# Performance work log

Hardware: AMD Instinct MI355X
Metric: run time of the kernel (lower is better)

Reference implementation:

```python
import jax, jax.numpy as jnp
import numpy as np

HID = 256
NUM_ENT = 100000
NUM_REL = 50
E = 320000  # edges per direction; edge_index has 2*E columns
BN_EPS = 1e-5


def setup_inputs() -> dict:
    key = jax.random.key(0)
    ks = jax.random.split(key, 10)
    x = jax.random.normal(ks[0], (NUM_ENT, HID), dtype=jnp.float32)
    edge_index = jax.random.randint(ks[1], (2, 2 * E), 0, NUM_ENT)
    edge_type = jax.random.randint(ks[2], (2 * E,), 0, NUM_REL)
    rel_embed = jax.random.normal(ks[3], (NUM_REL, HID), dtype=jnp.float32)
    # xavier_normal init: std = sqrt(2 / (fan_in + fan_out))
    w_std = (2.0 / (HID + HID)) ** 0.5
    w_loop = jax.random.normal(ks[4], (HID, HID), dtype=jnp.float32) * w_std
    w_in = jax.random.normal(ks[5], (HID, HID), dtype=jnp.float32) * w_std
    w_out = jax.random.normal(ks[6], (HID, HID), dtype=jnp.float32) * w_std
    w_rel = jax.random.normal(ks[7], (HID, HID), dtype=jnp.float32) * w_std
    loop_rel = jax.random.normal(ks[8], (1, HID), dtype=jnp.float32) * ((2.0 / (1 + HID)) ** 0.5)
    bn_weight = jnp.ones((HID,), dtype=jnp.float32)
    bn_bias = jnp.zeros((HID,), dtype=jnp.float32)
    return {
        "x": x, "edge_index": edge_index, "edge_type": edge_type,
        "rel_embed": rel_embed, "w_loop": w_loop, "w_in": w_in,
        "w_out": w_out, "w_rel": w_rel, "loop_rel": loop_rel,
        "bn_weight": bn_weight, "bn_bias": bn_bias,
    }


def _compute_norm(edge_index, num_ent):
    # symmetric D^-1/2 * D^-1/2 norm; degree counted on row (target) index
    row, col = edge_index[0], edge_index[1]
    deg = jax.ops.segment_sum(jnp.ones_like(row, dtype=jnp.float32), row, num_segments=num_ent)
    deg_inv = jnp.where(deg > 0, deg ** -0.5, 0.0)
    return deg_inv[row] * deg_inv[col]


def _propagate(x, idx, etype, rel_all, W, norm, num_ent):
    # gather source nodes (idx[1]), compose with relation emb (mult), transform, scale, scatter-add to targets (idx[0])
    msg = (x[idx[1]] * rel_all[etype]) @ W  # [E, d]
    if norm is not None:
        msg = msg * norm[:, None]
    return jax.ops.segment_sum(msg, idx[0], num_segments=num_ent)


def reference(x, edge_index, edge_type, rel_embed, w_loop, w_in, w_out, w_rel,
              loop_rel, bn_weight, bn_bias):
    num_ent = x.shape[0]
    rel_all = jnp.concatenate([rel_embed, loop_rel], axis=0)  # [R+1, d]
    e = edge_index.shape[1] // 2
    in_index, out_index = edge_index[:, :e], edge_index[:, e:]
    in_type, out_type = edge_type[:e], edge_type[e:]

    in_norm = _compute_norm(in_index, num_ent)
    out_norm = _compute_norm(out_index, num_ent)

    in_res = _propagate(x, in_index, in_type, rel_all, w_in, in_norm, num_ent)
    out_res = _propagate(x, out_index, out_type, rel_all, w_out, out_norm, num_ent)
    # self-loop: identity scatter -> just per-node compose+transform
    loop_res = (x * loop_rel) @ w_loop

    out = (in_res + out_res + loop_res) * (1.0 / 3.0)

    # BatchNorm1d in training mode (batch stats, biased variance)
    mean = out.mean(axis=0)
    var = out.var(axis=0)
    out = (out - mean) * jax.lax.rsqrt(var + BN_EPS) * bn_weight + bn_bias

    rel_out = (rel_all @ w_rel)[:-1]  # drop loop relation
    return out, rel_out
```

## Files before the change

### kernel.cpp

```cpp
#include <hip/hip_runtime.h>

#define HID     256
#define N_ENT   100000
#define TOT_E   640000
#define HALF_E  320000
#define NSEG    (2 * N_ENT)
#define BN_EPSF 1e-5f
#define SCAN_ELEMS 1024
#define NBLK_SCAN  ((NSEG + SCAN_ELEMS - 1) / SCAN_ELEMS)

typedef short bf16x8 __attribute__((ext_vector_type(8)));
typedef short bf16x4 __attribute__((ext_vector_type(4)));
typedef float f32x4  __attribute__((ext_vector_type(4)));

__device__ __forceinline__ short f2b(float f) {
    union { float f; unsigned u; } c; c.f = f;
    unsigned u = c.u;
    u += 0x7FFF + ((u >> 16) & 1);
    return (short)(u >> 16);
}
__device__ __forceinline__ float b2f(short b) {
    union { unsigned u; float f; } c;
    c.u = ((unsigned)(unsigned short)b) << 16;
    return c.f;
}

#define NX8 (N_ENT * HID / 8)
#define NR8 (50 * HID / 8)
#define CONV_BLOCKS ((NX8 + NR8 + 255) / 256)
__global__ void prep_kernel(const float* __restrict__ x, short* __restrict__ xh,
                            const float* __restrict__ rel, short* __restrict__ relh,
                            const float* __restrict__ w_in, const float* __restrict__ w_out,
                            const float* __restrict__ w_loop, const float* __restrict__ loop_rel,
                            short* __restrict__ WT,
                            int* __restrict__ offs, float* __restrict__ stats) {
    int bid = blockIdx.x;
    int tid = threadIdx.x;
    if (bid < CONV_BLOCKS) {
        int i = bid * 256 + tid;
        if (i < NSEG) offs[i] = 0;
        if (i < 512) stats[i] = 0.f;
        const float* src; short* dst; int idx;
        if (i < NX8) { src = x; dst = xh; idx = i; }
        else if (i < NX8 + NR8) { src = rel; dst = relh; idx = i - NX8; }
        else return;
        const float4* p = (const float4*)(src + (size_t)idx * 8);
        float4 v0 = p[0], v1 = p[1];
        bf16x8 pk;
        pk[0]=f2b(v0.x); pk[1]=f2b(v0.y); pk[2]=f2b(v0.z); pk[3]=f2b(v0.w);
        pk[4]=f2b(v1.x); pk[5]=f2b(v1.y); pk[6]=f2b(v1.z); pk[7]=f2b(v1.w);
        *(bf16x8*)(dst + (size_t)idx * 8) = pk;
    } else {
        int n = bid - CONV_BLOCKS;
        int t = tid;
        float v0 = w_in  [(size_t)t * HID + n];
        float v1 = w_out [(size_t)t * HID + n];
        float v2 = w_loop[(size_t)t * HID + n] * loop_rel[t];
        short* row = WT + (size_t)n * 768;
        row[t]       = f2b(v0);
        row[256 + t] = f2b(v1);
        row[512 + t] = f2b(v2);
    }
}

__global__ void hist_kernel(const int* __restrict__ ei, int* __restrict__ offs) {
    int j = blockIdx.x * 256 + threadIdx.x;
    if (j >= TOT_E) return;
    int seg = ei[j] + ((j < HALF_E) ? 0 : N_ENT);
    atomicAdd(&offs[seg], 1);
}

__global__ __launch_bounds__(256) void scan1(int* __restrict__ offs, int* __restrict__ bsums,
                                             float* __restrict__ rnorm) {
    __shared__ int tsum[256];
    int b = blockIdx.x, t = threadIdx.x;
    int base = b * SCAN_ELEMS + t * 4;
    int v[4] = {0, 0, 0, 0};
    if (base + 3 < NSEG) {
        int4 lv = *(const int4*)(offs + base);
        v[0] = lv.x; v[1] = lv.y; v[2] = lv.z; v[3] = lv.w;
    } else {
        for (int i = 0; i < 4; ++i) if (base + i < NSEG) v[i] = offs[base + i];
    }
    #pragma unroll
    for (int i = 0; i < 4; ++i)
        if (base + i < NSEG)
            rnorm[base + i] = (v[i] > 0) ? rsqrtf((float)v[i]) : 0.f;
    tsum[t] = v[0] + v[1] + v[2] + v[3];
    __syncthreads();
    for (int d = 1; d < 256; d <<= 1) {
        int val = (t >= d) ? tsum[t - d] : 0;
        __syncthreads();
        tsum[t] += val;
        __syncthreads();
    }
    int run = (t == 0) ? 0 : tsum[t - 1];
    if (t == 255) bsums[b] = tsum[255];
    int w[4];
    for (int i = 0; i < 4; ++i) { w[i] = run; run += v[i]; }
    if (base + 3 < NSEG) *(int4*)(offs + base) = make_int4(w[0], w[1], w[2], w[3]);
    else for (int i = 0; i < 4; ++i) if (base + i < NSEG) offs[base + i] = w[i];
}

__global__ __launch_bounds__(256) void scan3f(int* __restrict__ offs, const int* __restrict__ bsums) {
    __shared__ int tmp[256];
    int b = blockIdx.x, t = threadIdx.x;
    tmp[t] = (t < NBLK_SCAN) ? bsums[t] : 0;
    __syncthreads();
    for (int d = 1; d < 256; d <<= 1) {
        int val = (t >= d) ? tmp[t - d] : 0;
        __syncthreads();
        tmp[t] += val;
        __syncthreads();
    }
    int add = (b == 0) ? 0 : tmp[b - 1];
    int base = b * SCAN_ELEMS + t * 4;
    if (base + 3 < NSEG) {
        int4 v = *(int4*)(offs + base);
        v.x += add; v.y += add; v.z += add; v.w += add;
        *(int4*)(offs + base) = v;
    } else {
        for (int i = 0; i < 4; ++i) if (base + i < NSEG) offs[base + i] += add;
    }
}

__global__ void fill8_kernel(const int* __restrict__ ei, const int* __restrict__ et,
                             int* __restrict__ offs, const float* __restrict__ rnorm,
                             int2* __restrict__ elist8) {
    int j = blockIdx.x * 256 + threadIdx.x;
    if (j >= TOT_E) return;
    int hb  = (j < HALF_E) ? 0 : N_ENT;
    int seg = ei[j] + hb;
    int col = ei[TOT_E + j];
    float norm = rnorm[seg] * rnorm[hb + col];
    int pos = atomicAdd(&offs[seg], 1);
    elist8[pos] = make_int2(col | (et[j] << 17), __float_as_int(norm));
}

__global__ __launch_bounds__(256) void gather_h(
        const short* __restrict__ xh, const short* __restrict__ relh,
        const int* __restrict__ offs, const int2* __restrict__ elist8,
        short* __restrict__ accA, short* __restrict__ accB) {
    int s = blockIdx.x * 4 + (threadIdx.x >> 6);
    int lane = threadIdx.x & 63;
    int start = (s == 0) ? 0 : offs[s - 1];
    int end   = offs[s];
    float ax0=0.f, ay0=0.f, az0=0.f, aw0=0.f;
    float ax1=0.f, ay1=0.f, az1=0.f, aw1=0.f;
    int e = start;
    for (; e + 2 <= end; e += 2) {
        int2 p0 = elist8[e];
        int2 p1 = elist8[e + 1];
        int   c0 = p0.x & 0x1FFFF, t0 = p0.x >> 17;
        float n0 = __int_as_float(p0.y);
        int   c1 = p1.x & 0x1FFFF, t1 = p1.x >> 17;
        float n1 = __int_as_float(p1.y);
        bf16x4 xv0 = *(const bf16x4*)(xh   + (size_t)c0 * HID + lane * 4);
        bf16x4 rv0 = *(const bf16x4*)(relh + (size_t)t0 * HID + lane * 4);
        bf16x4 xv1 = *(const bf16x4*)(xh   + (size_t)c1 * HID + lane * 4);
        bf16x4 rv1 = *(const bf16x4*)(relh + (size_t)t1 * HID + lane * 4);
        ax0 += b2f(xv0[0]) * b2f(rv0[0]) * n0;
        ay0 += b2f(xv0[1]) * b2f(rv0[1]) * n0;
        az0 += b2f(xv0[2]) * b2f(rv0[2]) * n0;
        aw0 += b2f(xv0[3]) * b2f(rv0[3]) * n0;
        ax1 += b2f(xv1[0]) * b2f(rv1[0]) * n1;
        ay1 += b2f(xv1[1]) * b2f(rv1[1]) * n1;
        az1 += b2f(xv1[2]) * b2f(rv1[2]) * n1;
        aw1 += b2f(xv1[3]) * b2f(rv1[3]) * n1;
    }
    if (e < end) {
        int2 p = elist8[e];
        int   c = p.x & 0x1FFFF, t = p.x >> 17;
        float n = __int_as_float(p.y);
        bf16x4 xv = *(const bf16x4*)(xh   + (size_t)c * HID + lane * 4);
        bf16x4 rv = *(const bf16x4*)(relh + (size_t)t * HID + lane * 4);
        ax0 += b2f(xv[0]) * b2f(rv[0]) * n;
        ay0 += b2f(xv[1]) * b2f(rv[1]) * n;
        az0 += b2f(xv[2]) * b2f(rv[2]) * n;
        aw0 += b2f(xv[3]) * b2f(rv[3]) * n;
    }
    int hb = (s >= N_ENT) ? N_ENT : 0;
    short* dst = ((s >= N_ENT) ? accB : accA) + (size_t)(s - hb) * HID + lane * 4;
    bf16x4 pk;
    pk[0] = f2b(ax0 + ax1); pk[1] = f2b(ay0 + ay1);
    pk[2] = f2b(az0 + az1); pk[3] = f2b(aw0 + aw1);
    *(bf16x4*)dst = pk;
}

template <bool BF16OUT>
__global__ __launch_bounds__(256, 4) void gemm_mfma_h(
        const short* __restrict__ accA, const short* __restrict__ accB,
        const short* __restrict__ xh, const short* __restrict__ WT,
        float* __restrict__ out, short* __restrict__ outh, float* __restrict__ stats)
{
    __shared__ __align__(16) short As[64 * 64];
    __shared__ __align__(16) short Bs[256 * 64];
    const int tid = threadIdx.x;
    const int l   = tid & 63;
    const int wid = tid >> 6;
    const int r0  = blockIdx.x * 64;
    const int lr  = l & 15;
    const int lg  = l >> 4;

    f32x4 acc[4][4];
    #pragma unroll
    for (int i = 0; i < 4; ++i)
        #pragma unroll
        for (int j = 0; j < 4; ++j)
            acc[i][j] = (f32x4){0.f, 0.f, 0.f, 0.f};

    const int sg = tid & 7;
    const int sr = tid >> 3;

    for (int kt = 0; kt < 12; ++kt) {
        const int src = kt >> 2;
        const short* Ap = (src == 0) ? accA : ((src == 1) ? accB : xh);
        const int ksg = kt * 64;
        const int ksl = (kt & 3) * 64;
        __syncthreads();
        #pragma unroll
        for (int h = 0; h < 2; ++h) {
            int r  = sr + 32 * h;
            int gr = r0 + r;
            bf16x8 v = {0,0,0,0,0,0,0,0};
            if (gr < N_ENT) v = *(const bf16x8*)(Ap + (size_t)gr * HID + ksl + sg * 8);
            *(bf16x8*)&As[r * 64 + ((sg ^ (r & 7)) << 3)] = v;
        }
        #pragma unroll
        for (int i = 0; i < 8; ++i) {
            int n = sr + 32 * i;
            bf16x8 w = *(const bf16x8*)(WT + (size_t)n * 768 + ksg + sg * 8);
            *(bf16x8*)&Bs[n * 64 + ((sg ^ (n & 7)) << 3)] = w;
        }
        __syncthreads();
        #pragma unroll
        for (int kc = 0; kc < 2; ++kc) {
            const int gsel = kc * 4 + lg;
            bf16x8 af[4];
            #pragma unroll
            for (int i = 0; i < 4; ++i) {
                int r = 16 * i + lr;
                af[i] = *(const bf16x8*)&As[r * 64 + ((gsel ^ (r & 7)) << 3)];
            }
            #pragma unroll
            for (int j = 0; j < 4; ++j) {
                int n = wid * 64 + 16 * j + lr;
                bf16x8 bfr = *(const bf16x8*)&Bs[n * 64 + ((gsel ^ (n & 7)) << 3)];
                #pragma unroll
                for (int i = 0; i < 4; ++i)
                    acc[i][j] = __builtin_amdgcn_mfma_f32_16x16x32_bf16(
                                    af[i], bfr, acc[i][j], 0, 0, 0);
            }
        }
    }

    const float third = 1.f / 3.f;
    float s[4]  = {0.f, 0.f, 0.f, 0.f};
    float sq[4] = {0.f, 0.f, 0.f, 0.f};
    #pragma unroll
    for (int i = 0; i < 4; ++i) {
        #pragma unroll
        for (int v = 0; v < 4; ++v) {
            int grow = r0 + 16 * i + lg * 4 + v;
            if (grow < N_ENT) {
                #pragma unroll
                for (int j = 0; j < 4; ++j) {
                    float val = acc[i][j][v] * third;
                    int col = wid * 64 + 16 * j + lr;
                    if (BF16OUT) outh[(size_t)grow * HID + col] = f2b(val);
                    else         out [(size_t)grow * HID + col] = val;
                    s[j] += val; sq[j] += val * val;
                }
            }
        }
    }
    #pragma unroll
    for (int j = 0; j < 4; ++j) {
        s[j]  += __shfl_xor(s[j], 16);  s[j]  += __shfl_xor(s[j], 32);
        sq[j] += __shfl_xor(sq[j], 16); sq[j] += __shfl_xor(sq[j], 32);
    }
    if (lg == 0) {
        #pragma unroll
        for (int j = 0; j < 4; ++j) {
            int c = wid * 64 + 16 * j + lr;
            atomicAdd(&stats[c], s[j]);
            atomicAdd(&stats[HID + c], sq[j]);
        }
    }
}

#define BN_BLOCKS 1024
__global__ void bn_relout_h(const short* __restrict__ outh, float* __restrict__ out,
                            const float* __restrict__ stats,
                            const float* __restrict__ bnw, const float* __restrict__ bnb,
                            const float* __restrict__ rel_embed, const float* __restrict__ w_rel,
                            float* __restrict__ rel_out) {
    if (blockIdx.x < BN_BLOCKS) {
        const float invN = 1.f / (float)N_ENT;
        const int total8 = N_ENT * (HID / 8);
        for (int i = blockIdx.x * 256 + threadIdx.x; i < total8; i += BN_BLOCKS * 256) {
            int c = (i & 31) * 8;
            bf16x8 v = *(const bf16x8*)(outh + (size_t)i * 8);
            float r[8];
            #pragma unroll
            for (int k = 0; k < 8; ++k) {
                float mean = stats[c + k] * invN;
                float var  = stats[HID + c + k] * invN - mean * mean;
                float sc   = rsqrtf(var + BN_EPSF) * bnw[c + k];
                float sh   = bnb[c + k] - mean * sc;
                r[k] = b2f(v[k]) * sc + sh;
            }
            float4* dst = (float4*)(out + (size_t)i * 8);
            dst[0] = make_float4(r[0], r[1], r[2], r[3]);
            dst[1] = make_float4(r[4], r[5], r[6], r[7]);
        }
    } else {
        __shared__ float row[HID];
        int r = blockIdx.x - BN_BLOCKS;
        int c = threadIdx.x;
        row[c] = rel_embed[(size_t)r * HID + c];
        __syncthreads();
        float sum = 0.f;
        #pragma unroll 8
        for (int k = 0; k < HID; ++k) sum += row[k] * w_rel[(size_t)k * HID + c];
        rel_out[(size_t)r * HID + c] = sum;
    }
}

__global__ void bn_relout_f(float* __restrict__ out, const float* __restrict__ stats,
                            const float* __restrict__ bnw, const float* __restrict__ bnb,
                            const float* __restrict__ rel_embed, const float* __restrict__ w_rel,
                            float* __restrict__ rel_out) {
    if (blockIdx.x < BN_BLOCKS) {
        const float invN = 1.f / (float)N_ENT;
        const int total4 = N_ENT * (HID / 4);
        for (int i = blockIdx.x * 256 + threadIdx.x; i < total4; i += BN_BLOCKS * 256) {
            int c = (i & 63) * 4;
            float4 v = *(float4*)(out + (size_t)i * 4);
            #pragma unroll
            for (int k = 0; k < 4; ++k) {
                float mean = stats[c + k] * invN;
                float var  = stats[HID + c + k] * invN - mean * mean;
                float sc   = rsqrtf(var + BN_EPSF) * bnw[c + k];
                float sh   = bnb[c + k] - mean * sc;
                float* comp = (k == 0) ? &v.x : (k == 1) ? &v.y : (k == 2) ? &v.z : &v.w;
                *comp = (*comp) * sc + sh;
            }
            *(float4*)(out + (size_t)i * 4) = v;
        }
    } else {
        __shared__ float row[HID];
        int r = blockIdx.x - BN_BLOCKS;
        int c = threadIdx.x;
        row[c] = rel_embed[(size_t)r * HID + c];
        __syncthreads();
        float sum = 0.f;
        #pragma unroll 8
        for (int k = 0; k < HID; ++k) sum += row[k] * w_rel[(size_t)k * HID + c];
        rel_out[(size_t)r * HID + c] = sum;
    }
}

extern "C" void kernel_launch(void* const* d_in, const int* in_sizes, int n_in,
                              void* d_out, int out_size, void* d_ws, size_t ws_size,
                              hipStream_t stream) {
    const float* x        = (const float*)d_in[0];
    const int*   ei       = (const int*)d_in[1];
    const int*   et       = (const int*)d_in[2];
    const float* rel      = (const float*)d_in[3];
    const float* w_loop   = (const float*)d_in[4];
    const float* w_in     = (const float*)d_in[5];
    const float* w_out    = (const float*)d_in[6];
    const float* w_rel    = (const float*)d_in[7];
    const float* loop_rel = (const float*)d_in[8];
    const float* bnw      = (const float*)d_in[9];
    const float* bnb      = (const float*)d_in[10];

    float* out     = (float*)d_out;
    float* rel_out = out + (size_t)N_ENT * HID;

    const size_t XH_B   = (size_t)N_ENT * HID * 2;
    const size_t ACC_B  = (size_t)N_ENT * HID * 2;
    const size_t OFFS_B = (size_t)NSEG * 4;
    const size_t EL8_B  = (size_t)TOT_E * 8;
    const size_t RN_B   = (size_t)NSEG * 4;
    const size_t RELH_B = (size_t)50 * HID * 2;
    const size_t WT_B   = (size_t)256 * 768 * 2;
    const size_t base_need = XH_B + 2 * ACC_B + OFFS_B + EL8_B + RN_B
                           + 256 * 4 + 512 * 4 + RELH_B + WT_B;
    const size_t OUTH_B = (size_t)N_ENT * HID * 2;
    const bool   have_outh = (ws_size >= base_need + OUTH_B);

    char* w = (char*)d_ws;
    short* xh     = (short*)w;              w += XH_B;
    short* accA_h = (short*)w;              w += ACC_B;
    short* accB_h = (short*)w;              w += ACC_B;
    int*   offs   = (int*)w;                w += OFFS_B;
    int2*  elist8 = (int2*)w;               w += EL8_B;
    float* rnorm  = (float*)w;              w += RN_B;
    int*   bsums  = (int*)w;                w += 256 * 4;
    float* stats  = (float*)w;              w += 512 * 4;
    short* relh   = (short*)w;              w += RELH_B;
    short* WT     = (short*)w;              w += WT_B;
    short* outh   = (short*)w;

    prep_kernel<<<CONV_BLOCKS + 256, 256, 0, stream>>>(x, xh, rel, relh,
                                                       w_in, w_out, w_loop, loop_rel,
                                                       WT, offs, stats);
    hist_kernel<<<TOT_E / 256, 256, 0, stream>>>(ei, offs);
    scan1<<<NBLK_SCAN, 256, 0, stream>>>(offs, bsums, rnorm);
    scan3f<<<NBLK_SCAN, 256, 0, stream>>>(offs, bsums);
    fill8_kernel<<<TOT_E / 256, 256, 0, stream>>>(ei, et, offs, rnorm, elist8);
    gather_h<<<NSEG / 4, 256, 0, stream>>>(xh, relh, offs, elist8, accA_h, accB_h);
    if (have_outh) {
        gemm_mfma_h<true><<<(N_ENT + 63) / 64, 256, 0, stream>>>(
            accA_h, accB_h, xh, WT, out, outh, stats);
        bn_relout_h<<<BN_BLOCKS + 50, 256, 0, stream>>>(outh, out, stats, bnw, bnb,
                                                        rel, w_rel, rel_out);
    } else {
        gemm_mfma_h<false><<<(N_ENT + 63) / 64, 256, 0, stream>>>(
            accA_h, accB_h, xh, WT, out, outh, stats);
        bn_relout_f<<<BN_BLOCKS + 50, 256, 0, stream>>>(out, stats, bnw, bnb,
                                                        rel, w_rel, rel_out);
    }
}
```

Before: 375.4 us.

## Fuse edge gather-aggregate into MFMA GEMM via shared-memory A tiles

Merges the separate gather kernel into the GEMM kernel. Each block now aggregates the in and out messages for its 64 rows directly into a 64x256 shared-memory tile, then runs the MFMA GEMM against that tile, phase by phase. This drops the two bf16 intermediate accumulator buffers and one launch, saving a full write and read of them through global memory. In exchange, shared memory per block grows to about 64 KB and the gather phase serialises 16 rows per wave, which reduces occupancy and the latency hiding available to the irregular gathers.

```diff
diff --git a/kernel.cpp b/kernel.cpp
--- a/kernel.cpp
+++ b/kernel.cpp
@@ -137,63 +137,14 @@
     elist8[pos] = make_int2(col | (et[j] << 17), __float_as_int(norm));
 }
 
-__global__ __launch_bounds__(256) void gather_h(
+template <bool BF16OUT>
+__global__ __launch_bounds__(256) void fused_gg(
         const short* __restrict__ xh, const short* __restrict__ relh,
         const int* __restrict__ offs, const int2* __restrict__ elist8,
-        short* __restrict__ accA, short* __restrict__ accB) {
-    int s = blockIdx.x * 4 + (threadIdx.x >> 6);
-    int lane = threadIdx.x & 63;
-    int start = (s == 0) ? 0 : offs[s - 1];
-    int end   = offs[s];
-    float ax0=0.f, ay0=0.f, az0=0.f, aw0=0.f;
-    float ax1=0.f, ay1=0.f, az1=0.f, aw1=0.f;
-    int e = start;
-    for (; e + 2 <= end; e += 2) {
-        int2 p0 = elist8[e];
-        int2 p1 = elist8[e + 1];
-        int   c0 = p0.x & 0x1FFFF, t0 = p0.x >> 17;
-        float n0 = __int_as_float(p0.y);
-        int   c1 = p1.x & 0x1FFFF, t1 = p1.x >> 17;
-        float n1 = __int_as_float(p1.y);
-        bf16x4 xv0 = *(const bf16x4*)(xh   + (size_t)c0 * HID + lane * 4);
-        bf16x4 rv0 = *(const bf16x4*)(relh + (size_t)t0 * HID + lane * 4);
-        bf16x4 xv1 = *(const bf16x4*)(xh   + (size_t)c1 * HID + lane * 4);
-        bf16x4 rv1 = *(const bf16x4*)(relh + (size_t)t1 * HID + lane * 4);
-        ax0 += b2f(xv0[0]) * b2f(rv0[0]) * n0;
-        ay0 += b2f(xv0[1]) * b2f(rv0[1]) * n0;
-        az0 += b2f(xv0[2]) * b2f(rv0[2]) * n0;
-        aw0 += b2f(xv0[3]) * b2f(rv0[3]) * n0;
-        ax1 += b2f(xv1[0]) * b2f(rv1[0]) * n1;
-        ay1 += b2f(xv1[1]) * b2f(rv1[1]) * n1;
-        az1 += b2f(xv1[2]) * b2f(rv1[2]) * n1;
-        aw1 += b2f(xv1[3]) * b2f(rv1[3]) * n1;
-    }
-    if (e < end) {
-        int2 p = elist8[e];
-        int   c = p.x & 0x1FFFF, t = p.x >> 17;
-        float n = __int_as_float(p.y);
-        bf16x4 xv = *(const bf16x4*)(xh   + (size_t)c * HID + lane * 4);
-        bf16x4 rv = *(const bf16x4*)(relh + (size_t)t * HID + lane * 4);
-        ax0 += b2f(xv[0]) * b2f(rv[0]) * n;
-        ay0 += b2f(xv[1]) * b2f(rv[1]) * n;
-        az0 += b2f(xv[2]) * b2f(rv[2]) * n;
-        aw0 += b2f(xv[3]) * b2f(rv[3]) * n;
-    }
-    int hb = (s >= N_ENT) ? N_ENT : 0;
-    short* dst = ((s >= N_ENT) ? accB : accA) + (size_t)(s - hb) * HID + lane * 4;
-    bf16x4 pk;
-    pk[0] = f2b(ax0 + ax1); pk[1] = f2b(ay0 + ay1);
-    pk[2] = f2b(az0 + az1); pk[3] = f2b(aw0 + aw1);
-    *(bf16x4*)dst = pk;
-}
-
-template <bool BF16OUT>
-__global__ __launch_bounds__(256, 4) void gemm_mfma_h(
-        const short* __restrict__ accA, const short* __restrict__ accB,
-        const short* __restrict__ xh, const short* __restrict__ WT,
+        const short* __restrict__ WT,
         float* __restrict__ out, short* __restrict__ outh, float* __restrict__ stats)
 {
-    __shared__ __align__(16) short As[64 * 64];
+    __shared__ __align__(16) short As[64 * 256];
     __shared__ __align__(16) short Bs[256 * 64];
     const int tid = threadIdx.x;
     const int l   = tid & 63;
@@ -201,6 +152,8 @@
     const int r0  = blockIdx.x * 64;
     const int lr  = l & 15;
     const int lg  = l >> 4;
+    const int sg  = tid & 7;
+    const int sr  = tid >> 3;
 
     f32x4 acc[4][4];
     #pragma unroll
@@ -209,48 +162,105 @@
         for (int j = 0; j < 4; ++j)
             acc[i][j] = (f32x4){0.f, 0.f, 0.f, 0.f};
 
-    const int sg = tid & 7;
-    const int sr = tid >> 3;
-
-    for (int kt = 0; kt < 12; ++kt) {
-        const int src = kt >> 2;
-        const short* Ap = (src == 0) ? accA : ((src == 1) ? accB : xh);
-        const int ksg = kt * 64;
-        const int ksl = (kt & 3) * 64;
-        __syncthreads();
-        #pragma unroll
-        for (int h = 0; h < 2; ++h) {
-            int r  = sr + 32 * h;
-            int gr = r0 + r;
-            bf16x8 v = {0,0,0,0,0,0,0,0};
-            if (gr < N_ENT) v = *(const bf16x8*)(Ap + (size_t)gr * HID + ksl + sg * 8);
-            *(bf16x8*)&As[r * 64 + ((sg ^ (r & 7)) << 3)] = v;
-        }
-        #pragma unroll
-        for (int i = 0; i < 8; ++i) {
-            int n = sr + 32 * i;
-            bf16x8 w = *(const bf16x8*)(WT + (size_t)n * 768 + ksg + sg * 8);
-            *(bf16x8*)&Bs[n * 64 + ((sg ^ (n & 7)) << 3)] = w;
-        }
-        __syncthreads();
-        #pragma unroll
-        for (int kc = 0; kc < 2; ++kc) {
-            const int gsel = kc * 4 + lg;
-            bf16x8 af[4];
+    for (int phase = 0; phase < 3; ++phase) {
+        if (phase < 2) {
+            const int hb = (phase == 0) ? 0 : N_ENT;
+            #pragma unroll 1
+            for (int rr = 0; rr < 16; ++rr) {
+                const int r  = wid * 16 + rr;
+                const int gr = r0 + r;
+                float ax0=0.f, ay0=0.f, az0=0.f, aw0=0.f;
+                float ax1=0.f, ay1=0.f, az1=0.f, aw1=0.f;
+                if (gr < N_ENT) {
+                    int seg   = hb + gr;
+                    int start = (seg == 0) ? 0 : offs[seg - 1];
+                    int end   = offs[seg];
+                    int e = start;
+                    for (; e + 2 <= end; e += 2) {
+                        int2 p0 = elist8[e];
+                        int2 p1 = elist8[e + 1];
+                        int   c0 = p0.x & 0x1FFFF, t0 = p0.x >> 17;
+                        float n0 = __int_as_float(p0.y);
+                        int   c1 = p1.x & 0x1FFFF, t1 = p1.x >> 17;
+                        float n1 = __int_as_float(p1.y);
+                        bf16x4 xv0 = *(const bf16x4*)(xh   + (size_t)c0 * HID + l * 4);
+                        bf16x4 rv0 = *(const bf16x4*)(relh + (size_t)t0 * HID + l * 4);
+                        bf16x4 xv1 = *(const bf16x4*)(xh   + (size_t)c1 * HID + l * 4);
+                        bf16x4 rv1 = *(const bf16x4*)(relh + (size_t)t1 * HID + l * 4);
+                        ax0 += b2f(xv0[0]) * b2f(rv0[0]) * n0;
+                        ay0 += b2f(xv0[1]) * b2f(rv0[1]) * n0;
+                        az0 += b2f(xv0[2]) * b2f(rv0[2]) * n0;
+                        aw0 += b2f(xv0[3]) * b2f(rv0[3]) * n0;
+                        ax1 += b2f(xv1[0]) * b2f(rv1[0]) * n1;
+                        ay1 += b2f(xv1[1]) * b2f(rv1[1]) * n1;
+                        az1 += b2f(xv1[2]) * b2f(rv1[2]) * n1;
+                        aw1 += b2f(xv1[3]) * b2f(rv1[3]) * n1;
+                    }
+                    if (e < end) {
+                        int2 p = elist8[e];
+                        int   c = p.x & 0x1FFFF, t = p.x >> 17;
+                        float n = __int_as_float(p.y);
+                        bf16x4 xv = *(const bf16x4*)(xh   + (size_t)c * HID + l * 4);
+                        bf16x4 rv = *(const bf16x4*)(relh + (size_t)t * HID + l * 4);
+                        ax0 += b2f(xv[0]) * b2f(rv[0]) * n;
+                        ay0 += b2f(xv[1]) * b2f(rv[1]) * n;
+                        az0 += b2f(xv[2]) * b2f(rv[2]) * n;
+                        aw0 += b2f(xv[3]) * b2f(rv[3]) * n;
+                    }
+                }
+                int g    = l >> 1;
+                int slot = (g & 24) | ((g ^ r) & 7);
+                bf16x4 pk;
+                pk[0] = f2b(ax0 + ax1); pk[1] = f2b(ay0 + ay1);
+                pk[2] = f2b(az0 + az1); pk[3] = f2b(aw0 + aw1);
+                *(bf16x4*)&As[r * 256 + slot * 8 + (l & 1) * 4] = pk;
+            }
+        } else {
             #pragma unroll
-            for (int i = 0; i < 4; ++i) {
-                int r = 16 * i + lr;
-                af[i] = *(const bf16x8*)&As[r * 64 + ((gsel ^ (r & 7)) << 3)];
-            }
+            for (int h = 0; h < 2; ++h) {
+                int r  = sr + 32 * h;
+                int gr = r0 + r;
+                #pragma unroll
+                for (int c = 0; c < 4; ++c) {
+                    bf16x8 v = {0,0,0,0,0,0,0,0};
+                    if (gr < N_ENT)
+                        v = *(const bf16x8*)(xh + (size_t)gr * HID + (c * 8 + sg) * 8);
+                    int slot = c * 8 + ((sg ^ r) & 7);
+                    *(bf16x8*)&As[r * 256 + slot * 8] = v;
+                }
+            }
+        }
+        __syncthreads();
+
+        for (int ktl = 0; ktl < 4; ++ktl) {
+            const int ksg = phase * 256 + ktl * 64;
             #pragma unroll
-            for (int j = 0; j < 4; ++j) {
-                int n = wid * 64 + 16 * j + lr;
-                bf16x8 bfr = *(const bf16x8*)&Bs[n * 64 + ((gsel ^ (n & 7)) << 3)];
+            for (int i = 0; i < 8; ++i) {
+                int n = sr + 32 * i;
+                bf16x8 w = *(const bf16x8*)(WT + (size_t)n * 768 + ksg + sg * 8);
+                *(bf16x8*)&Bs[n * 64 + ((sg ^ (n & 7)) << 3)] = w;
+            }
+            __syncthreads();
+            #pragma unroll
+            for (int kc = 0; kc < 2; ++kc) {
+                const int gsel = kc * 4 + lg;
+                bf16x8 af[4];
                 #pragma unroll
-                for (int i = 0; i < 4; ++i)
-                    acc[i][j] = __builtin_amdgcn_mfma_f32_16x16x32_bf16(
-                                    af[i], bfr, acc[i][j], 0, 0, 0);
-            }
+                for (int i = 0; i < 4; ++i) {
+                    int r = 16 * i + lr;
+                    af[i] = *(const bf16x8*)&As[r * 256 + (ktl * 8 + ((gsel ^ r) & 7)) * 8];
+                }
+                #pragma unroll
+                for (int j = 0; j < 4; ++j) {
+                    int n = wid * 64 + 16 * j + lr;
+                    bf16x8 bfr = *(const bf16x8*)&Bs[n * 64 + ((gsel ^ (n & 7)) << 3)];
+                    #pragma unroll
+                    for (int i = 0; i < 4; ++i)
+                        acc[i][j] = __builtin_amdgcn_mfma_f32_16x16x32_bf16(
+                                        af[i], bfr, acc[i][j], 0, 0, 0);
+                }
+            }
+            __syncthreads();
         }
     }
 
@@ -380,21 +390,18 @@
     float* rel_out = out + (size_t)N_ENT * HID;
 
     const size_t XH_B   = (size_t)N_ENT * HID * 2;
-    const size_t ACC_B  = (size_t)N_ENT * HID * 2;
     const size_t OFFS_B = (size_t)NSEG * 4;
     const size_t EL8_B  = (size_t)TOT_E * 8;
     const size_t RN_B   = (size_t)NSEG * 4;
     const size_t RELH_B = (size_t)50 * HID * 2;
     const size_t WT_B   = (size_t)256 * 768 * 2;
-    const size_t base_need = XH_B + 2 * ACC_B + OFFS_B + EL8_B + RN_B
+    const size_t base_need = XH_B + OFFS_B + EL8_B + RN_B
                            + 256 * 4 + 512 * 4 + RELH_B + WT_B;
     const size_t OUTH_B = (size_t)N_ENT * HID * 2;
     const bool   have_outh = (ws_size >= base_need + OUTH_B);
 
     char* w = (char*)d_ws;
     short* xh     = (short*)w;              w += XH_B;
-    short* accA_h = (short*)w;              w += ACC_B;
-    short* accB_h = (short*)w;              w += ACC_B;
     int*   offs   = (int*)w;                w += OFFS_B;
     int2*  elist8 = (int2*)w;               w += EL8_B;
     float* rnorm  = (float*)w;              w += RN_B;
@@ -411,15 +418,14 @@
     scan1<<<NBLK_SCAN, 256, 0, stream>>>(offs, bsums, rnorm);
     scan3f<<<NBLK_SCAN, 256, 0, stream>>>(offs, bsums);
     fill8_kernel<<<TOT_E / 256, 256, 0, stream>>>(ei, et, offs, rnorm, elist8);
-    gather_h<<<NSEG / 4, 256, 0, stream>>>(xh, relh, offs, elist8, accA_h, accB_h);
     if (have_outh) {
-        gemm_mfma_h<true><<<(N_ENT + 63) / 64, 256, 0, stream>>>(
-            accA_h, accB_h, xh, WT, out, outh, stats);
+        fused_gg<true><<<(N_ENT + 63) / 64, 256, 0, stream>>>(
+            xh, relh, offs, elist8, WT, out, outh, stats);
         bn_relout_h<<<BN_BLOCKS + 50, 256, 0, stream>>>(outh, out, stats, bnw, bnb,
                                                         rel, w_rel, rel_out);
     } else {
-        gemm_mfma_h<false><<<(N_ENT + 63) / 64, 256, 0, stream>>>(
-            accA_h, accB_h, xh, WT, out, outh, stats);
+        fused_gg<false><<<(N_ENT + 63) / 64, 256, 0, stream>>>(
+            xh, relh, offs, elist8, WT, out, outh, stats);
         bn_relout_f<<<BN_BLOCKS + 50, 256, 0, stream>>>(out, stats, bnw, bnb,
                                                         rel, w_rel, rel_out);
     }
```

After: 412.9 us. 10.0% more time.
